# Kernel tuning notes

Hardware: AMD Instinct MI355X
Metric: run time of the kernel (lower is better)

Reference implementation:

```python
import jax, jax.numpy as jnp
import numpy as np

B, C, T = 4, 80, 800            # batch, n_mels (= d_model), frames
DEPTH, D_IN, N, DT_R, K = 12, 160, 16, 5, 4  # layers, expand*d_model, d_state, dt_rank, conv kernel
ATT, EMB, EPS = 128, 192, 1e-12

LP_NAMES = ['ln1_g','ln1_b','in_proj','conv_w','conv_b','x_proj','dt_w','dt_b','A_log','D','out_proj','ln2_g','ln2_b','ff_w1','ff_b1','ff_w2','ff_b2']
PP_NAMES = ['att_w1','att_b1','bn1_g','bn1_b','bn1_m','bn1_v','att_w2','att_b2','bn2_g','bn2_b','bn2_m','bn2_v','fc_w','fc_b']


def _layernorm(x, g, b, eps=1e-5):
    mu = x.mean(-1, keepdims=True)
    v = ((x - mu) ** 2).mean(-1, keepdims=True)
    return (x - mu) * jax.lax.rsqrt(v + eps) * g + b


def _mamba(x, p):
    # x: [B, L, d_model] -> standard Mamba selective-scan block
    xz = x @ p['in_proj']                              # [B,L,2*D_IN]
    xc, z = jnp.split(xz, 2, axis=-1)
    xp = jnp.pad(xc, ((0, 0), (K - 1, 0), (0, 0)))     # causal left pad
    xc = jax.lax.conv_general_dilated(
        xp, p['conv_w'], (1,), 'VALID',
        dimension_numbers=('NWC', 'WIO', 'NWC'),
        feature_group_count=D_IN) + p['conv_b']
    xc = jax.nn.silu(xc)
    dbc = xc @ p['x_proj']                             # [B,L,DT_R+2N]
    dt, Bm, Cm = jnp.split(dbc, [DT_R, DT_R + N], axis=-1)
    dt = jax.nn.softplus(dt @ p['dt_w'] + p['dt_b'])   # [B,L,D_IN]
    A = -jnp.exp(p['A_log'])                           # [D_IN,N]

    def step(h, inp):
        x_t, dt_t, B_t, C_t = inp                      # [B,D],[B,D],[B,N],[B,N]
        dA = jnp.exp(dt_t[..., None] * A)              # [B,D,N]
        h = dA * h + (dt_t * x_t)[..., None] * B_t[:, None, :]
        y = jnp.einsum('bdn,bn->bd', h, C_t)
        return h, y

    h0 = jnp.zeros((x.shape[0], D_IN, N), x.dtype)
    xs = tuple(jnp.swapaxes(a, 0, 1) for a in (xc, dt, Bm, Cm))
    _, ys = jax.lax.scan(step, h0, xs)
    y = jnp.swapaxes(ys, 0, 1) + xc * p['D']
    y = y * jax.nn.silu(z)
    return y @ p['out_proj']


def _encoder(x, p):
    xn = _layernorm(x, p['ln1_g'], p['ln1_b'])
    fwd = _mamba(xn, p)
    bwd = jnp.flip(_mamba(jnp.flip(xn, 1), p), 1)      # bidirectional, shared weights
    m = _layernorm(fwd + bwd, p['ln2_g'], p['ln2_b'])
    ff = jax.nn.gelu(m @ p['ff_w1'] + p['ff_b1'], approximate=False) @ p['ff_w2'] + p['ff_b2']
    return ff + x


def _forward(feat, lp, pp):
    feat = feat - feat.mean(-1, keepdims=True)         # CMN
    x = jnp.swapaxes(feat, 1, 2)                       # [B,T,C]

    def body(xc, p):
        return _encoder(xc, p), None

    x, _ = jax.lax.scan(body, x, lp)                   # 12 stacked layers
    x = jnp.swapaxes(x, 1, 2)                          # [B,C,T]

    # Attentive statistics pooling (global context)
    mean = x.mean(-1, keepdims=True)
    std = jnp.sqrt(jnp.maximum(((x - mean) ** 2).mean(-1, keepdims=True), EPS))
    g = jnp.concatenate([x, jnp.broadcast_to(mean, x.shape), jnp.broadcast_to(std, x.shape)], axis=1)  # [B,3C,T]
    a = jnp.einsum('bct,cd->bdt', g, pp['att_w1']) + pp['att_b1'][:, None]
    a = jax.nn.relu(a)
    a = (a - pp['bn1_m'][:, None]) * jax.lax.rsqrt(pp['bn1_v'][:, None] + 1e-5) * pp['bn1_g'][:, None] + pp['bn1_b'][:, None]
    a = jnp.tanh(a)
    a = jnp.einsum('bdt,dc->bct', a, pp['att_w2']) + pp['att_b2'][:, None]
    w = jax.nn.softmax(a, axis=-1)
    mu = jnp.sum(w * x, axis=-1)
    sg = jnp.sqrt(jnp.maximum(jnp.sum(w * x * x, axis=-1) - mu ** 2, EPS))
    pooled = jnp.concatenate([mu, sg], axis=-1)        # [B,2C]

    pooled = (pooled - pp['bn2_m']) * jax.lax.rsqrt(pp['bn2_v'] + 1e-5) * pp['bn2_g'] + pp['bn2_b']
    return pooled @ pp['fc_w'] + pp['fc_b']            # [B,EMB] source embedding


def setup_inputs() -> dict:
    key = jax.random.key(0)
    ks = jax.random.split(key, 12)

    def w(k, shape, s=0.05):
        return jax.random.normal(k, shape, jnp.float32) * s

    L = DEPTH
    return {
        'feat': jax.random.normal(ks[0], (B, C, T), jnp.float32),
        'ln1_g': jnp.ones((L, C)), 'ln1_b': jnp.zeros((L, C)),
        'in_proj': w(ks[1], (L, C, 2 * D_IN)),
        'conv_w': w(ks[2], (L, K, 1, D_IN), 0.2),
        'conv_b': jnp.zeros((L, D_IN)),
        'x_proj': w(ks[3], (L, D_IN, DT_R + 2 * N)),
        'dt_w': w(ks[4], (L, DT_R, D_IN), 0.2),
        'dt_b': jnp.full((L, D_IN), -2.0),
        'A_log': jnp.tile(jnp.log(jnp.arange(1, N + 1, dtype=jnp.float32)), (L, D_IN, 1)),
        'D': jnp.ones((L, D_IN)),
        'out_proj': w(ks[5], (L, D_IN, C)),
        'ln2_g': jnp.ones((L, C)), 'ln2_b': jnp.zeros((L, C)),
        'ff_w1': w(ks[6], (L, C, 4 * C)), 'ff_b1': jnp.zeros((L, 4 * C)),
        'ff_w2': w(ks[7], (L, 4 * C, C)), 'ff_b2': jnp.zeros((L, C)),
        'att_w1': w(ks[8], (3 * C, ATT)), 'att_b1': jnp.zeros((ATT,)),
        'bn1_g': jnp.ones((ATT,)), 'bn1_b': jnp.zeros((ATT,)),
        'bn1_m': jnp.zeros((ATT,)), 'bn1_v': jnp.ones((ATT,)),
        'att_w2': w(ks[9], (ATT, C)), 'att_b2': jnp.zeros((C,)),
        'bn2_g': jnp.ones((2 * C,)), 'bn2_b': jnp.zeros((2 * C,)),
        'bn2_m': jnp.zeros((2 * C,)), 'bn2_v': jnp.ones((2 * C,)),
        'fc_w': w(ks[10], (2 * C, EMB)), 'fc_b': jnp.zeros((EMB,)),
        'aug': 0,
    }


def reference(feat, ln1_g, ln1_b, in_proj, conv_w, conv_b, x_proj, dt_w, dt_b, A_log, D, out_proj, ln2_g, ln2_b, ff_w1, ff_b1, ff_w2, ff_b2, att_w1, att_b1, bn1_g, bn1_b, bn1_m, bn1_v, att_w2, att_b2, bn2_g, bn2_b, bn2_m, bn2_v, fc_w, fc_b, aug):
    lp = dict(zip(LP_NAMES, (ln1_g, ln1_b, in_proj, conv_w, conv_b, x_proj, dt_w, dt_b, A_log, D, out_proj, ln2_g, ln2_b, ff_w1, ff_b1, ff_w2, ff_b2)))
    pp = dict(zip(PP_NAMES, (att_w1, att_b1, bn1_g, bn1_b, bn1_m, bn1_v, att_w2, att_b2, bn2_g, bn2_b, bn2_m, bn2_v, fc_w, fc_b)))
    # aug == 0 -> SpecAug skipped (eval path); speaker branch (frozen, no_grad) omitted
    return _forward(feat, lp, pp)
```

## Files before the change

kernel.cpp:

```cpp
#include <hip/hip_runtime.h>
#include <hip/hip_bf16.h>

#define B_ 4
#define C_ 80
#define T_ 800
#define R_ 3200
#define DIN 160
#define NST 16
#define NC 16
#define LCH 50

typedef const float* fp;

__device__ __forceinline__ void g2l16(const float* g, float* l) {
  __builtin_amdgcn_global_load_lds(
      (const __attribute__((address_space(1))) void*)g,
      (__attribute__((address_space(3))) void*)l,
      16, 0, 0);
}

__device__ __forceinline__ float blockSum(float v, float* sb) {
  for (int o = 32; o; o >>= 1) v += __shfl_xor(v, o);
  __syncthreads();
  if ((threadIdx.x & 63) == 0) sb[threadIdx.x >> 6] = v;
  __syncthreads();
  return sb[0] + sb[1] + sb[2] + sb[3];
}
__device__ __forceinline__ float blockMax(float v, float* sb) {
  for (int o = 32; o; o >>= 1) v = fmaxf(v, __shfl_xor(v, o));
  __syncthreads();
  if ((threadIdx.x & 63) == 0) sb[threadIdx.x >> 6] = v;
  __syncthreads();
  return fmaxf(fmaxf(sb[0], sb[1]), fmaxf(sb[2], sb[3]));
}

__global__ __launch_bounds__(256) void prepw_k(fp in_proj, fp ff_w1,
    fp ln1_g, fp ln1_b, fp ln2_g, fp ln2_b, fp ff_b1,
    float* __restrict__ wp, float* __restrict__ uvb) {
  int idx = blockIdx.x * 256 + threadIdx.x;
  int c = idx % 320, lm = idx / 320;
  int mat = lm & 1, l = lm >> 1;
  fp W = (mat ? ff_w1 : in_proj) + l * 25600;
  fp g = (mat ? ln2_g : ln1_g) + l * 80;
  fp b = (mat ? ln2_b : ln1_b) + l * 80;
  float* wpo = wp + lm * 25600;
  float u = 0.f, v = 0.f;
  for (int k = 0; k < 80; ++k) {
    float w = W[k * 320 + c];
    float gw = g[k] * w;
    wpo[k * 320 + c] = gw;
    u += gw;
    v += b[k] * w;
  }
  if (mat) v += ff_b1[l * 320 + c];
  uvb[lm * 640 + c] = u;
  uvb[lm * 640 + 320 + c] = v;
}

__global__ __launch_bounds__(256) void prepx_k(fp x_proj, float* __restrict__ xpt) {
  int idx = blockIdx.x * 256 + threadIdx.x;
  if (idx >= 71040) return;
  int l = idx / 5920, r = idx % 5920;
  int c = r / 160, k = r % 160;
  xpt[idx] = x_proj[l * 5920 + k * 37 + c];
}

__global__ __launch_bounds__(256) void prept_k(fp out_proj, fp ff_w2,
    float* __restrict__ wot, float* __restrict__ w2t) {
  int idx = blockIdx.x * 256 + threadIdx.x;
  if (idx < 153600) {
    int l = idx / 12800, r = idx % 12800;
    int c = r / 160, k = r % 160;
    wot[idx] = out_proj[l * 12800 + k * 80 + c];
  } else if (idx < 153600 + 307200) {
    int j = idx - 153600;
    int l = j / 25600, r = j % 25600;
    int c = r / 320, k = r % 320;
    w2t[j] = ff_w2[l * 25600 + k * 80 + c];
  }
}

__global__ __launch_bounds__(256) void cmn_k(fp feat, float* __restrict__ x) {
  int bc = blockIdx.x;
  int b = bc / C_, c = bc % C_;
// ... 34 lines not shown
    float mu = s * 0.0125f;
    float rs = rsqrtf(fmaxf(q * 0.0125f - mu * mu, 0.f) + 1e-5f);
    must[row * 2] = mu;
    must[row * 2 + 1] = rs;
  }
}

template<int EPI>
__global__ __launch_bounds__(256, 4) void gw_k(const float* __restrict__ A,
    fp W, fp uv, const float* __restrict__ must, const float* __restrict__ extra,
    float* __restrict__ out, int N) {
  __shared__ float SL[5120 + 4 * 1280];
  int tid = threadIdx.x, wv = tid >> 6, ln = tid & 63;
  int bid = blockIdx.x;
  int c0 = (bid / 50) * 64;
  int row0 = ((bid % 50) * 4 + wv) * 16;
  for (int ch = wv; ch < 20; ch += 4) {
    int m = ch * 256 + ln * 4;
    int kr = m >> 6, cc = m & 63;
    int lo = __builtin_amdgcn_readfirstlane(ch * 256);
    g2l16(W + kr * N + c0 + cc, SL + lo);
  }
  int abase = __builtin_amdgcn_readfirstlane(5120 + wv * 1280);
  float* As = SL + 5120 + wv * 1280;
  #pragma unroll
  for (int i = 0; i < 5; ++i) {
    int m = i * 256 + ln * 4;
    int r = m / 80, kk = m - r * 80;
    g2l16(A + (row0 + r) * 80 + kk, SL + abase + i * 256);
  }
  __syncthreads();
  int rq = ln >> 4, c16 = ln & 15;
  float acc[4][4] = {};
  #pragma unroll 2
  for (int k4 = 0; k4 < 80; k4 += 4) {
    float4 a[4], w[4];
    #pragma unroll
    for (int i = 0; i < 4; ++i)
      a[i] = *(const float4*)&As[(rq * 4 + i) * 80 + k4];
    #pragma unroll
    for (int kk = 0; kk < 4; ++kk)
      w[kk] = *(const float4*)&SL[(k4 + kk) * 64 + c16 * 4];
    #pragma unroll
    for (int i = 0; i < 4; ++i) {
      acc[i][0] += a[i].x*w[0].x + a[i].y*w[1].x + a[i].z*w[2].x + a[i].w*w[3].x;
      acc[i][1] += a[i].x*w[0].y + a[i].y*w[1].y + a[i].z*w[2].y + a[i].w*w[3].y;
      acc[i][2] += a[i].x*w[0].z + a[i].y*w[1].z + a[i].z*w[2].z + a[i].w*w[3].z;
      acc[i][3] += a[i].x*w[0].w + a[i].y*w[1].w + a[i].z*w[2].w + a[i].w*w[3].w;
    }
  }
  float ua[4], va[4];
  if (EPI != 3) {
    *(float4*)ua = *(const float4*)&uv[c0 + c16 * 4];
    *(float4*)va = *(const float4*)&uv[N + c0 + c16 * 4];
  }
  #pragma unroll
  for (int i = 0; i < 4; ++i) {
    int row = row0 + rq * 4 + i;
    float mu = 0.f, rs = 1.f;
    if (EPI != 3) {
      float2 ms = *(const float2*)&must[row * 2];
      mu = ms.x; rs = ms.y;
    }
    float4 o;
    float* op = &o.x;
    #pragma unroll
    for (int j = 0; j < 4; ++j) {
      float v = acc[i][j];
      if (EPI == 3) {
        int c = c0 + c16 * 4 + j;
        v += extra[(row / T_) * 128 + c];
        v = fmaxf(v, 0.f);
        v = v * extra[512 + c] + extra[640 + c];
        v = tanhf(v);
      } else {
        v = rs * v - mu * rs * ua[j] + va[j];
      }
      op[j] = v;
    }
    *(float4*)&out[row * N + c0 + c16 * 4] = o;
  }
}

template<int EPI, int KCH, int NKC, int SUM2, int STAT>
__global__ __launch_bounds__(256, 4) void gc_k(const float* __restrict__ A,
    fp W, fp bias, const float* __restrict__ extra, float* __restrict__ out,
    int Astride, float* __restrict__ must) {
  constexpr int P = KCH + 4;
  __shared__ float As[16 * P];
  __shared__ float Wt[80 * P];
  int tid = threadIdx.x;
  int row0 = blockIdx.x * 16;
  int rr = tid >> 4, c16 = tid & 15;
  float acc[5] = {};
  for (int kc = 0; kc < NKC; ++kc) {
    if (kc) __syncthreads();
    #pragma unroll
    for (int i = 0; i < 16 * KCH / 256; ++i) {
      int e = tid + i * 256;
      int r = e / KCH, k = e - r * KCH;
      float v;
      if (SUM2) v = A[(row0 + r) * 320 + k] + A[(row0 + r) * 320 + 160 + k];
      else      v = A[(row0 + r) * Astride + kc * KCH + k];
      As[r * P + k] = v;
    }
    #pragma unroll
    for (int i = 0; i < KCH * 80 / 256; ++i) {
      int e = tid + i * 256;
      int kr = e / 80, c = e - kr * 80;
      Wt[c * P + kr] = W[(kc * KCH + kr) * 80 + c];
    }
    __syncthreads();
    #pragma unroll 4
    for (int k4 = 0; k4 < KCH; k4 += 4) {
      float4 a = *(const float4*)&As[rr * P + k4];
      #pragma unroll
      for (int m = 0; m < 5; ++m) {
        float4 w = *(const float4*)&Wt[(c16 + 16 * m) * P + k4];
        acc[m] += a.x * w.x + a.y * w.y + a.z * w.z + a.w * w.w;
      }
    }
  }
  int row = row0 + rr;
  #pragma unroll
  for (int m = 0; m < 5; ++m) {
    int c = c16 + 16 * m;
    float v = acc[m];
    if (EPI == 2) v += bias[c] + extra[row * 80 + c];
    else if (EPI == 4) v += bias[c];
    out[row * 80 + c] = v;
  }
}

__global__ __launch_bounds__(256, 2) void gof_k(const float* __restrict__ yg,
    fp wotl, fp w1pl, fp uv1, float* __restrict__ g1) {
  __shared__ float As[16 * 164];
  __shared__ float Wt[80 * 164];
  __shared__ float sl[16 * 84];
  __shared__ float ss[32];
  int tid = threadIdx.x, row0 = blockIdx.x * 16, rr = tid >> 4, c16 = tid & 15;
  #pragma unroll
  for (int i = 0; i < 10; ++i) {
    int e = tid + i * 256; int r = e / 160, k = e - r * 160;
    As[r * 164 + k] = yg[(row0 + r) * 320 + k] + yg[(row0 + r) * 320 + 160 + k];
  }
  #pragma unroll
  for (int i = 0; i < 50; ++i) {
    int e = tid + i * 256; int c = e / 160, k = e - c * 160;
    Wt[c * 164 + k] = wotl[e];
  }
  __syncthreads();
  float acc[5] = {};
  #pragma unroll 4
  for (int k4 = 0; k4 < 160; k4 += 4) {
    float4 a = *(const float4*)&As[rr * 164 + k4];
    #pragma unroll
    for (int m = 0; m < 5; ++m) {
      float4 w = *(const float4*)&Wt[(c16 + 16 * m) * 164 + k4];
      acc[m] += a.x * w.x + a.y * w.y + a.z * w.z + a.w * w.w;
    }
  }
  float s = 0.f, q = 0.f;
  #pragma unroll
  for (int m = 0; m < 5; ++m) {
    float v = acc[m];
    sl[rr * 84 + c16 + 16 * m] = v;
    s += v; q += v * v;
  }
  s += __shfl_xor(s, 1); s += __shfl_xor(s, 2);
  s += __shfl_xor(s, 4); s += __shfl_xor(s, 8);
  q += __shfl_xor(q, 1); q += __shfl_xor(q, 2);
  q += __shfl_xor(q, 4); q += __shfl_xor(q, 8);
  if (c16 == 0) {
    float mu = s * 0.0125f;
    ss[rr * 2] = mu;
    ss[rr * 2 + 1] = rsqrtf(fmaxf(q * 0.0125f - mu * mu, 0.f) + 1e-5f);
  }
  for (int h = 0; h < 2; ++h) {
    __syncthreads();
    #pragma unroll
    for (int i = 0; i < 50; ++i) {
      int e = tid + i * 256; int kr = e / 160, c = e - kr * 160;
      Wt[kr * 164 + c] = w1pl[kr * 320 + h * 160 + c];
    }
    __syncthreads();
    float mu = ss[rr * 2], rs = ss[rr * 2 + 1];
    float a2[10] = {};
    for (int k = 0; k < 80; k += 4) {
      float4 av = *(const float4*)&sl[rr * 84 + k];
      #pragma unroll
      for (int m = 0; m < 10; ++m) {
        int c = c16 + 16 * m;
        a2[m] += av.x * Wt[k * 164 + c] + av.y * Wt[(k + 1) * 164 + c]
               + av.z * Wt[(k + 2) * 164 + c] + av.w * Wt[(k + 3) * 164 + c];
      }
    }
    #pragma unroll
    for (int m = 0; m < 10; ++m) {
      int c = h * 160 + c16 + 16 * m;
      float v = rs * a2[m] - mu * rs * uv1[c] + uv1[320 + c];
      v = 0.5f * v * (1.f + erff(v * 0.70710678118f));
      g1[(row0 + rr) * 320 + c] = v;
    }
  }
}

template<int LAST>
__global__ __launch_bounds__(256, 2) void gfi_k(const float* __restrict__ g1,
    fp w2tl, fp fb2, float* __restrict__ x, fp wpn, fp uvn,
    float* __restrict__ xz) {
  __shared__ float As[16 * 164];
  __shared__ float Wt[80 * 164];
  __shared__ float xn[16 * 84];
  __shared__ float ss[32];
  int tid = threadIdx.x, row0 = blockIdx.x * 16, rr = tid >> 4, c16 = tid & 15;
  float acc[5] = {};
  for (int kc = 0; kc < 2; ++kc) {
    if (kc) __syncthreads();
    #pragma unroll
    for (int i = 0; i < 10; ++i) {
      int e = tid + i * 256; int r = e / 160, k = e - r * 160;
      As[r * 164 + k] = g1[(row0 + r) * 320 + kc * 160 + k];
    }
    #pragma unroll
    for (int i = 0; i < 50; ++i) {
      int e = tid + i * 256; int c = e / 160, k = e - c * 160;
      Wt[c * 164 + k] = w2tl[c * 320 + kc * 160 + k];
    }
    __syncthreads();
    #pragma unroll 4
    for (int k4 = 0; k4 < 160; k4 += 4) {
      float4 a = *(const float4*)&As[rr * 164 + k4];
      #pragma unroll
      for (int m = 0; m < 5; ++m) {
        float4 w = *(const float4*)&Wt[(c16 + 16 * m) * 164 + k4];
        acc[m] += a.x * w.x + a.y * w.y + a.z * w.z + a.w * w.w;
      }
    }
  }
  float s = 0.f, q = 0.f;
  #pragma unroll
  for (int m = 0; m < 5; ++m) {
    int c = c16 + 16 * m;
    float v = acc[m] + fb2[c] + x[(row0 + rr) * 80 + c];
    x[(row0 + rr) * 80 + c] = v;
    xn[rr * 84 + c] = v;
    s += v; q += v * v;
  }
  if (!LAST) {
    s += __shfl_xor(s, 1); s += __shfl_xor(s, 2);
    s += __shfl_xor(s, 4); s += __shfl_xor(s, 8);
    q += __shfl_xor(q, 1); q += __shfl_xor(q, 2);
    q += __shfl_xor(q, 4); q += __shfl_xor(q, 8);
    if (c16 == 0) {
      float mu = s * 0.0125f;
      ss[rr * 2] = mu;
      ss[rr * 2 + 1] = rsqrtf(fmaxf(q * 0.0125f - mu * mu, 0.f) + 1e-5f);
    }
    for (int h = 0; h < 2; ++h) {
      __syncthreads();
      #pragma unroll
      for (int i = 0; i < 50; ++i) {
        int e = tid + i * 256; int kr = e / 160, c = e - kr * 160;
        Wt[kr * 164 + c] = wpn[kr * 320 + h * 160 + c];
      }
      __syncthreads();
      float mu = ss[rr * 2], rs = ss[rr * 2 + 1];
      float a2[10] = {};
      for (int k = 0; k < 80; k += 4) {
        float4 av = *(const float4*)&xn[rr * 84 + k];
        #pragma unroll
        for (int m = 0; m < 10; ++m) {
          int c = c16 + 16 * m;
          a2[m] += av.x * Wt[k * 164 + c] + av.y * Wt[(k + 1) * 164 + c]
                 + av.z * Wt[(k + 2) * 164 + c] + av.w * Wt[(k + 3) * 164 + c];
        }
      }
      #pragma unroll
      for (int m = 0; m < 10; ++m) {
        int c = h * 160 + c16 + 16 * m;
        xz[(row0 + rr) * 320 + c] = rs * a2[m] - mu * rs * uvn[c] + uvn[320 + c];
      }
    }
  }
}

__global__ __launch_bounds__(256) void cxf_k(const float* __restrict__ xz,
    fp cw, fp cb, fp xptl, fp dtw, fp dtb,
    float* __restrict__ xcf, float* __restrict__ xcbb,
    float* __restrict__ dbc2, float* __restrict__ dt2) {
  __shared__ float As[16 * 164];
  __shared__ float xpT[37 * 164];
  __shared__ float dbcl[16 * 40];
  int bi = blockIdx.x;
  int tc = bi % 50; int rem = bi / 50;
  int b = rem & 3, dir = rem >> 2;
  int t0 = tc * 16;
  int tid = threadIdx.x;
  #pragma unroll
  for (int i = 0; i < 24; ++i) {
    int e = tid + i * 256;
    if (e < 5920) {
      int c = e / 160, k = e - c * 160;
      xpT[c * 164 + k] = xptl[e];
    }
  }
  float* xco = dir ? xcbb : xcf;
  #pragma unroll
  for (int i = 0; i < 3; ++i) {
    int e = tid + i * 256;
    if (e < 640) {
      int ii = e / 40, d4 = (e - ii * 40) * 4;
      int t = t0 + ii;
      float4 acc = *(const float4*)&cb[d4];
      #pragma unroll
      for (int k = 0; k < 4; ++k) {
        int tt = t - 3 + k;
        if (tt >= 0) {
          int src = dir ? (T_ - 1 - tt) : tt;
          float4 xv = *(const float4*)&xz[(b * T_ + src) * 320 + d4];
          float4 wv = *(const float4*)&cw[k * DIN + d4];
          acc.x += wv.x * xv.x; acc.y += wv.y * xv.y;
          acc.z += wv.z * xv.z; acc.w += wv.w * xv.w;
        }
      }
      float4 o;
      o.x = acc.x / (1.f + __expf(-acc.x));
      o.y = acc.y / (1.f + __expf(-acc.y));
      o.z = acc.z / (1.f + __expf(-acc.z));
      o.w = acc.w / (1.f + __expf(-acc.w));
      *(float4*)&As[ii * 164 + d4] = o;
      *(float4*)&xco[(b * T_ + t) * DIN + d4] = o;
    }
  }
  __syncthreads();
  int rr = tid >> 4, c16 = tid & 15;
  int grow0 = dir * R_ + b * T_ + t0;
  {
    float a0 = 0.f, a1 = 0.f, a2 = 0.f;
    for (int k4 = 0; k4 < 160; k4 += 4) {
      float4 a = *(const float4*)&As[rr * 164 + k4];
      float4 w0 = *(const float4*)&xpT[c16 * 164 + k4];
      float4 w1 = *(const float4*)&xpT[(c16 + 16) * 164 + k4];
      a0 += a.x * w0.x + a.y * w0.y + a.z * w0.z + a.w * w0.w;
      a1 += a.x * w1.x + a.y * w1.y + a.z * w1.z + a.w * w1.w;
      if (c16 < 5) {
        float4 w2 = *(const float4*)&xpT[(c16 + 32) * 164 + k4];
        a2 += a.x * w2.x + a.y * w2.y + a.z * w2.z + a.w * w2.w;
      }
    }
    dbcl[rr * 40 + c16] = a0;
    dbcl[rr * 40 + c16 + 16] = a1;
    dbc2[(grow0 + rr) * 37 + c16] = a0;
    dbc2[(grow0 + rr) * 37 + c16 + 16] = a1;
    if (c16 < 5) {
      dbcl[rr * 40 + c16 + 32] = a2;
      dbc2[(grow0 + rr) * 37 + c16 + 32] = a2;
    }
  }
  __syncthreads();
  #pragma unroll
  for (int i = 0; i < 10; ++i) {
    int e = tid + i * 256;
    int ii = e / 160, d = e - ii * 160;
    float v = dtb[d];
    #pragma unroll
    for (int m = 0; m < 5; ++m) v += dbcl[ii * 40 + m] * dtw[m * DIN + d];
    v = fmaxf(v, 0.f) + __logf(1.f + __expf(-fabsf(v)));
    dt2[(grow0 + ii) * DIN + d] = v;
  }
}

__global__ __launch_bounds__(256) void scanA_k(const float* __restrict__ dt2,
    const float* __restrict__ xcf, const float* __restrict__ xcbb,
    const float* __restrict__ dbc2, fp A_log,
    float* __restrict__ hend, float* __restrict__ pprod) {
  int bi = blockIdx.x;
  int cch = bi % NC; int rem = bi / NC;
  int dblk = rem % 10; rem /= 10;
  int b = rem % 4; int dir = rem / 4;
  int d0 = dblk * 16;
  int tid = threadIdx.x, dl = tid >> 4, n = tid & 15;
  int d = d0 + dl;
  float Areg = -__expf(A_log[d * NST + n]);
  __shared__ float sdt[LCH][16], sdx[LCH][16], sB[LCH][16];
  const float* xc = dir ? xcbb : xcf;
  int rbase = dir * R_ + b * T_ + cch * LCH;
  int rloc0 = b * T_ + cch * LCH;
  for (int e = tid; e < LCH * 16; e += 256) {
    int i = e >> 4, jj = e & 15;
    int grow = rbase + i;
    float dtv = dt2[grow * DIN + d0 + jj];
    sdt[i][jj] = dtv;
    sdx[i][jj] = dtv * xc[(rloc0 + i) * DIN + d0 + jj];
    sB[i][jj]  = dbc2[grow * 37 + 5 + jj];
  }
  __syncthreads();
  float h = 0.f, dts = 0.f;
  #pragma unroll 2
  for (int i = 0; i < LCH; ++i) {
    float dtv = sdt[i][dl];
    float a = __expf(dtv * Areg);
    h = a * h + sdx[i][dl] * sB[i][n];
    dts += dtv;
  }
  hend[bi * 256 + tid] = h;
  pprod[bi * 256 + tid] = __expf(dts * Areg);
}

__global__ __launch_bounds__(256) void scanC_k(const float* __restrict__ dt2,
    const float* __restrict__ dbc2, const float* __restrict__ xcf,
    const float* __restrict__ xcbb, const float* __restrict__ xz,
    fp A_log, fp Dp, const float* __restrict__ hend,
    const float* __restrict__ pprod, float* __restrict__ ygcat) {
  int bi = blockIdx.x;
  int cch = bi % NC; int rem = bi / NC;
  int dblk = rem % 10; rem /= 10;
  int b = rem % 4; int dir = rem / 4;
  int d0 = dblk * 16;
  int tid = threadIdx.x, dl = tid >> 4, n = tid & 15;
  int d = d0 + dl;
  float Areg = -__expf(A_log[d * NST + n]);
  __shared__ float sdt[LCH][16], sdx[LCH][16], sB[LCH][16], sC[LCH][16];
  __shared__ float sY[LCH][16];
  const float* xc = dir ? xcbb : xcf;
  int rbase = dir * R_ + b * T_ + cch * LCH;
  int rloc0 = b * T_ + cch * LCH;
  int sbase = (bi / NC) * (NC * 256) + tid;
  float h = 0.f;
  #pragma unroll
  for (int cc = 0; cc < NC; ++cc) {
    float p = pprod[sbase + cc * 256];
    float e = hend[sbase + cc * 256];
    if (cc < cch) h = p * h + e;
  }
  for (int e = tid; e < LCH * 16; e += 256) {
    int i = e >> 4, jj = e & 15;
    int grow = rbase + i;
    float dtv = dt2[grow * DIN + d0 + jj];
    sdt[i][jj] = dtv;
    sdx[i][jj] = dtv * xc[(rloc0 + i) * DIN + d0 + jj];
    sB[i][jj]  = dbc2[grow * 37 + 5 + jj];
    sC[i][jj]  = dbc2[grow * 37 + 21 + jj];
  }
  __syncthreads();
  for (int i = 0; i < LCH; ++i) {
    float a = __expf(sdt[i][dl] * Areg);
    h = a * h + sdx[i][dl] * sB[i][n];
    float y = h * sC[i][n];
    y += __shfl_xor(y, 1);
    y += __shfl_xor(y, 2);
    y += __shfl_xor(y, 4);
    y += __shfl_xor(y, 8);
    if (n == 0) sY[i][dl] = y;
  }
  __syncthreads();
  for (int e = tid; e < LCH * 16; e += 256) {
    int i = e >> 4, jj = e & 15;
    int t = cch * LCH + i;
    int rloc = b * T_ + t;
    float xcv = xc[rloc * DIN + d0 + jj];
    int orow = dir ? (b * T_ + (T_ - 1 - t)) : rloc;
    float z = xz[orow * 320 + 160 + d0 + jj];
    float sg = 1.f / (1.f + __expf(-z));
    ygcat[orow * 320 + dir * 160 + d0 + jj] = (sY[i][jj] + xcv * Dp[d0 + jj]) * (z * sg);
  }
}

__global__ __launch_bounds__(256) void stats_k(const float* __restrict__ x,
                                               float* __restrict__ meanv, float* __restrict__ stdv) {
  int bc = blockIdx.x; int b = bc / C_, c = bc % C_;
  __shared__ float sb[4];
  int tid = threadIdx.x;
  float v[4]; float s = 0.f;
  #pragma unroll
  for (int i = 0; i < 4; ++i) {
    int t = tid + i * 256;
    v[i] = (t < T_) ? x[(b * T_ + t) * C_ + c] : 0.f;
    s += v[i];
  }
  s = blockSum(s, sb);
  float mu = s * (1.f / T_);
  float q = 0.f;
  #pragma unroll
  for (int i = 0; i < 4; ++i) {
    int t = tid + i * 256;
    if (t < T_) { float dd = v[i] - mu; q += dd * dd; }
  }
  q = blockSum(q, sb);
  if (tid == 0) { meanv[bc] = mu; stdv[bc] = sqrtf(fmaxf(q * (1.f / T_), 1e-12f)); }
}

__global__ __launch_bounds__(256) void prep_k(const float* __restrict__ meanv,
    const float* __restrict__ stdv, fp w1, fp ab1, fp g1p, fp b1p, fp m1p, fp v1p,
    float* __restrict__ pack) {
  int idx = blockIdx.x * 256 + threadIdx.x;
  if (idx < 512) {
    int b = idx / 128, dcol = idx % 128;
    float acc = ab1[dcol];
    for (int c = 0; c < C_; ++c) {
      acc += meanv[b * C_ + c] * w1[(C_ + c) * 128 + dcol];
      acc += stdv[b * C_ + c] * w1[(2 * C_ + c) * 128 + dcol];
    }
    pack[idx] = acc;
  } else if (idx < 640) {
    int dcol = idx - 512;
    float kv = g1p[dcol] * rsqrtf(v1p[dcol] + 1e-5f);
    pack[512 + dcol] = kv;
    pack[640 + dcol] = b1p[dcol] - m1p[dcol] * kv;
  }
}

__global__ __launch_bounds__(256) void pool_k(const float* __restrict__ x,
    const float* __restrict__ scores, fp g2, fp b2, fp m2, fp v2,
    float* __restrict__ pooledn) {
  int bc = blockIdx.x; int b = bc / C_, c = bc % C_;
  __shared__ float sb[4];
  int tid = threadIdx.x;
  float sv[4], xv[4];
  float mx = -1e30f;
  #pragma unroll
  for (int i = 0; i < 4; ++i) {
    int t = tid + i * 256;
    if (t < T_) { sv[i] = scores[(b * T_ + t) * C_ + c]; xv[i] = x[(b * T_ + t) * C_ + c]; }
    else { sv[i] = -1e30f; xv[i] = 0.f; }
    mx = fmaxf(mx, sv[i]);
  }
  mx = blockMax(mx, sb);
  float se = 0.f, sx = 0.f, sxx = 0.f;
  #pragma unroll
  for (int i = 0; i < 4; ++i) {
    float e = expf(sv[i] - mx);
    se += e; sx += e * xv[i]; sxx += e * xv[i] * xv[i];
  }
  se = blockSum(se, sb);
  sx = blockSum(sx, sb);
  sxx = blockSum(sxx, sb);
  if (tid == 0) {
    float mu = sx / se;
    float sg = sqrtf(fmaxf(sxx / se - mu * mu, 1e-12f));
    int j0 = c, j1 = C_ + c;
    pooledn[b * 160 + j0] = (mu - m2[j0]) * rsqrtf(v2[j0] + 1e-5f) * g2[j0] + b2[j0];
    pooledn[b * 160 + j1] = (sg - m2[j1]) * rsqrtf(v2[j1] + 1e-5f) * g2[j1] + b2[j1];
  }
}

__global__ __launch_bounds__(256) void fc_k(const float* __restrict__ pooledn, fp fw, fp fb,
                                            float* __restrict__ out) {
  int idx = blockIdx.x * 256 + threadIdx.x;
  if (idx >= 4 * 192) return;
  int b = idx / 192, e = idx % 192;
  float acc = fb[e];
  for (int i = 0; i < 160; ++i) acc += pooledn[b * 160 + i] * fw[i * 192 + e];
  out[idx] = acc;
}

extern "C" void kernel_launch(void* const* d_in, const int* in_sizes, int n_in,
                              void* d_out, int out_size, void* d_ws, size_t ws_size,
                              hipStream_t stream) {
  fp feat   = (fp)d_in[0];
  fp ln1_g  = (fp)d_in[1];  fp ln1_b  = (fp)d_in[2];
  fp in_proj= (fp)d_in[3];
  fp conv_w = (fp)d_in[4];  fp conv_b = (fp)d_in[5];
  fp x_proj = (fp)d_in[6];
  fp dt_w   = (fp)d_in[7];  fp dt_b   = (fp)d_in[8];
  fp A_log  = (fp)d_in[9];  fp Dp     = (fp)d_in[10];
  fp out_proj=(fp)d_in[11];
  fp ln2_g  = (fp)d_in[12]; fp ln2_b  = (fp)d_in[13];
  fp ff_w1  = (fp)d_in[14]; fp ff_b1  = (fp)d_in[15];
  fp ff_w2  = (fp)d_in[16]; fp ff_b2  = (fp)d_in[17];
  fp att_w1 = (fp)d_in[18]; fp att_b1 = (fp)d_in[19];
  fp bn1_g  = (fp)d_in[20]; fp bn1_b  = (fp)d_in[21];
  fp bn1_m  = (fp)d_in[22]; fp bn1_v  = (fp)d_in[23];
  fp att_w2 = (fp)d_in[24]; fp att_b2 = (fp)d_in[25];
  fp bn2_g  = (fp)d_in[26]; fp bn2_b  = (fp)d_in[27];
  fp bn2_m  = (fp)d_in[28]; fp bn2_v  = (fp)d_in[29];
  fp fc_w   = (fp)d_in[30]; fp fc_b   = (fp)d_in[31];

  float* ws   = (float*)d_ws;
  float* x    = ws;
  float* xz   = ws + 256000;
  float* xcf  = ws + 1280000;
  float* xcb  = ws + 1792000;
  float* dbc2 = ws + 2304000;
  float* dt2  = ws + 2540800;
  float* hend = ws + 3564800;
  float* pprod= ws + 3892480;
  float* ygcat= ws + 4220160;
  float* meanv= ws + 5244160;
  float* stdv = ws + 5244480;
  float* pack = ws + 5244800;
  float* pooledn = ws + 5245568;
  float* wp   = ws + 5246208;
  float* uvb  = ws + 5860608;
  float* mst_x= ws + 5875968;
  float* xpt  = ws + 5882368;
  float* wot  = ws + 5953408;
  float* w2t  = ws + 6107008;
  float* g1   = xz;
  float* a1b  = hend;
  float* sc   = dt2;

  prepw_k<<<30, 256, 0, stream>>>(in_proj, ff_w1, ln1_g, ln1_b, ln2_g, ln2_b,
                                  ff_b1, wp, uvb);
  prepx_k<<<278, 256, 0, stream>>>(x_proj, xpt);
  prept_k<<<1800, 256, 0, stream>>>(out_proj, ff_w2, wot, w2t);
  cmn_k<<<320, 256, 0, stream>>>(feat, x);
  rstat_k<<<200, 256, 0, stream>>>(x, mst_x);
  gw_k<0><<<250, 256, 0, stream>>>(x, wp, uvb, mst_x, nullptr, xz, 320);

  for (int l = 0; l < 12; ++l) {
    cxf_k<<<400, 256, 0, stream>>>(xz, conv_w + l * 640, conv_b + l * 160,
                                   xpt + l * 5920, dt_w + l * 800, dt_b + l * 160,
                                   xcf, xcb, dbc2, dt2);
    scanA_k<<<1280, 256, 0, stream>>>(dt2, xcf, xcb, dbc2, A_log + l * 2560, hend, pprod);
    scanC_k<<<1280, 256, 0, stream>>>(dt2, dbc2, xcf, xcb, xz, A_log + l * 2560,
                                      Dp + l * 160, hend, pprod, ygcat);
    gof_k<<<200, 256, 0, stream>>>(ygcat, wot + l * 12800, wp + (2 * l + 1) * 25600,
                                   uvb + (2 * l + 1) * 640, g1);
    if (l < 11)
      gfi_k<0><<<200, 256, 0, stream>>>(g1, w2t + l * 25600, ff_b2 + l * 80, x,
                                        wp + (2 * l + 2) * 25600,
                                        uvb + (2 * l + 2) * 640, xz);
    else
      gfi_k<1><<<200, 256, 0, stream>>>(g1, w2t + l * 25600, ff_b2 + l * 80, x,
                                        wp, uvb, xz);
  }

  stats_k<<<320, 256, 0, stream>>>(x, meanv, stdv);
  prep_k<<<3, 256, 0, stream>>>(meanv, stdv, att_w1, att_b1, bn1_g, bn1_b, bn1_m, bn1_v, pack);
  gw_k<3><<<100, 256, 0, stream>>>(x, att_w1, nullptr, nullptr, pack, a1b, 128);
  gc_k<4, 128, 1, 0, 0><<<200, 256, 0, stream>>>(a1b, att_w2, att_b2, nullptr, sc, 128, nullptr);
  pool_k<<<320, 256, 0, stream>>>(x, sc, bn2_g, bn2_b, bn2_m, bn2_v, pooledn);
  fc_k<<<3, 256, 0, stream>>>(pooledn, fc_w, fc_b, (float*)d_out);
}
```

Measured before the change: 1.262 ms.

## Fuse per-layer encoder kernels into a persistent cooperative megakernel with grid syncs

Replaces the five per-layer kernel launches (conv/x_proj, two scan passes, out-projection and FFN stages) across 12 layers with one cooperative persistent kernel of 400 blocks. Grid-wide barriers separate the phases, and the scan work items are strided over the resident blocks. The aim is to remove launch gaps and inter-kernel drain and fill overhead. In exchange, the scans run with fewer concurrent blocks and a single large LDS allocation, and a fallback path with separate kernels is kept for when the cooperative launch fails.

```diff
diff --git a/kernel.cpp b/kernel.cpp
--- a/kernel.cpp
+++ b/kernel.cpp
@@ -1,5 +1,8 @@
 #include <hip/hip_runtime.h>
 #include <hip/hip_bf16.h>
+#include <hip/hip_cooperative_groups.h>
+
+namespace cg = cooperative_groups;
 
 #define B_ 4
 #define C_ 80
@@ -200,10 +203,9 @@
   }
 }
 
-template<int EPI, int KCH, int NKC, int SUM2, int STAT>
+template<int EPI, int KCH, int NKC>
 __global__ __launch_bounds__(256, 4) void gc_k(const float* __restrict__ A,
-    fp W, fp bias, const float* __restrict__ extra, float* __restrict__ out,
-    int Astride, float* __restrict__ must) {
+    fp W, fp bias, float* __restrict__ out, int Astride) {
   constexpr int P = KCH + 4;
   __shared__ float As[16 * P];
   __shared__ float Wt[80 * P];
@@ -217,10 +219,7 @@
     for (int i = 0; i < 16 * KCH / 256; ++i) {
       int e = tid + i * 256;
       int r = e / KCH, k = e - r * KCH;
-      float v;
-      if (SUM2) v = A[(row0 + r) * 320 + k] + A[(row0 + r) * 320 + 160 + k];
-      else      v = A[(row0 + r) * Astride + kc * KCH + k];
-      As[r * P + k] = v;
+      As[r * P + k] = A[(row0 + r) * Astride + kc * KCH + k];
     }
     #pragma unroll
     for (int i = 0; i < KCH * 80 / 256; ++i) {
@@ -244,173 +243,19 @@
   for (int m = 0; m < 5; ++m) {
     int c = c16 + 16 * m;
     float v = acc[m];
-    if (EPI == 2) v += bias[c] + extra[row * 80 + c];
-    else if (EPI == 4) v += bias[c];
+    if (EPI == 4) v += bias[c];
     out[row * 80 + c] = v;
   }
 }
 
-__global__ __launch_bounds__(256, 2) void gof_k(const float* __restrict__ yg,
-    fp wotl, fp w1pl, fp uv1, float* __restrict__ g1) {
-  __shared__ float As[16 * 164];
-  __shared__ float Wt[80 * 164];
-  __shared__ float sl[16 * 84];
-  __shared__ float ss[32];
-  int tid = threadIdx.x, row0 = blockIdx.x * 16, rr = tid >> 4, c16 = tid & 15;
-  #pragma unroll
-  for (int i = 0; i < 10; ++i) {
-    int e = tid + i * 256; int r = e / 160, k = e - r * 160;
-    As[r * 164 + k] = yg[(row0 + r) * 320 + k] + yg[(row0 + r) * 320 + 160 + k];
-  }
-  #pragma unroll
-  for (int i = 0; i < 50; ++i) {
-    int e = tid + i * 256; int c = e / 160, k = e - c * 160;
-    Wt[c * 164 + k] = wotl[e];
-  }
-  __syncthreads();
-  float acc[5] = {};
-  #pragma unroll 4
-  for (int k4 = 0; k4 < 160; k4 += 4) {
-    float4 a = *(const float4*)&As[rr * 164 + k4];
-    #pragma unroll
-    for (int m = 0; m < 5; ++m) {
-      float4 w = *(const float4*)&Wt[(c16 + 16 * m) * 164 + k4];
-      acc[m] += a.x * w.x + a.y * w.y + a.z * w.z + a.w * w.w;
-    }
-  }
-  float s = 0.f, q = 0.f;
-  #pragma unroll
-  for (int m = 0; m < 5; ++m) {
-    float v = acc[m];
-    sl[rr * 84 + c16 + 16 * m] = v;
-    s += v; q += v * v;
-  }
-  s += __shfl_xor(s, 1); s += __shfl_xor(s, 2);
-  s += __shfl_xor(s, 4); s += __shfl_xor(s, 8);
-  q += __shfl_xor(q, 1); q += __shfl_xor(q, 2);
-  q += __shfl_xor(q, 4); q += __shfl_xor(q, 8);
-  if (c16 == 0) {
-    float mu = s * 0.0125f;
-    ss[rr * 2] = mu;
-    ss[rr * 2 + 1] = rsqrtf(fmaxf(q * 0.0125f - mu * mu, 0.f) + 1e-5f);
-  }
-  for (int h = 0; h < 2; ++h) {
-    __syncthreads();
-    #pragma unroll
-    for (int i = 0; i < 50; ++i) {
-      int e = tid + i * 256; int kr = e / 160, c = e - kr * 160;
-      Wt[kr * 164 + c] = w1pl[kr * 320 + h * 160 + c];
-    }
-    __syncthreads();
-    float mu = ss[rr * 2], rs = ss[rr * 2 + 1];
-    float a2[10] = {};
-    for (int k = 0; k < 80; k += 4) {
-      float4 av = *(const float4*)&sl[rr * 84 + k];
-      #pragma unroll
-      for (int m = 0; m < 10; ++m) {
-        int c = c16 + 16 * m;
-        a2[m] += av.x * Wt[k * 164 + c] + av.y * Wt[(k + 1) * 164 + c]
-               + av.z * Wt[(k + 2) * 164 + c] + av.w * Wt[(k + 3) * 164 + c];
-      }
-    }
-    #pragma unroll
-    for (int m = 0; m < 10; ++m) {
-      int c = h * 160 + c16 + 16 * m;
-      float v = rs * a2[m] - mu * rs * uv1[c] + uv1[320 + c];
-      v = 0.5f * v * (1.f + erff(v * 0.70710678118f));
-      g1[(row0 + rr) * 320 + c] = v;
-    }
-  }
-}
-
-template<int LAST>
-__global__ __launch_bounds__(256, 2) void gfi_k(const float* __restrict__ g1,
-    fp w2tl, fp fb2, float* __restrict__ x, fp wpn, fp uvn,
-    float* __restrict__ xz) {
-  __shared__ float As[16 * 164];
-  __shared__ float Wt[80 * 164];
-  __shared__ float xn[16 * 84];
-  __shared__ float ss[32];
-  int tid = threadIdx.x, row0 = blockIdx.x * 16, rr = tid >> 4, c16 = tid & 15;
-  float acc[5] = {};
-  for (int kc = 0; kc < 2; ++kc) {
-    if (kc) __syncthreads();
-    #pragma unroll
-    for (int i = 0; i < 10; ++i) {
-      int e = tid + i * 256; int r = e / 160, k = e - r * 160;
-      As[r * 164 + k] = g1[(row0 + r) * 320 + kc * 160 + k];
-    }
-    #pragma unroll
-    for (int i = 0; i < 50; ++i) {
-      int e = tid + i * 256; int c = e / 160, k = e - c * 160;
-      Wt[c * 164 + k] = w2tl[c * 320 + kc * 160 + k];
-    }
-    __syncthreads();
-    #pragma unroll 4
-    for (int k4 = 0; k4 < 160; k4 += 4) {
-      float4 a = *(const float4*)&As[rr * 164 + k4];
-      #pragma unroll
-      for (int m = 0; m < 5; ++m) {
-        float4 w = *(const float4*)&Wt[(c16 + 16 * m) * 164 + k4];
-        acc[m] += a.x * w.x + a.y * w.y + a.z * w.z + a.w * w.w;
-      }
-    }
-  }
-  float s = 0.f, q = 0.f;
-  #pragma unroll
-  for (int m = 0; m < 5; ++m) {
-    int c = c16 + 16 * m;
-    float v = acc[m] + fb2[c] + x[(row0 + rr) * 80 + c];
-    x[(row0 + rr) * 80 + c] = v;
-    xn[rr * 84 + c] = v;
-    s += v; q += v * v;
-  }
-  if (!LAST) {
-    s += __shfl_xor(s, 1); s += __shfl_xor(s, 2);
-    s += __shfl_xor(s, 4); s += __shfl_xor(s, 8);
-    q += __shfl_xor(q, 1); q += __shfl_xor(q, 2);
-    q += __shfl_xor(q, 4); q += __shfl_xor(q, 8);
-    if (c16 == 0) {
-      float mu = s * 0.0125f;
-      ss[rr * 2] = mu;
-      ss[rr * 2 + 1] = rsqrtf(fmaxf(q * 0.0125f - mu * mu, 0.f) + 1e-5f);
-    }
-    for (int h = 0; h < 2; ++h) {
-      __syncthreads();
-      #pragma unroll
-      for (int i = 0; i < 50; ++i) {
-        int e = tid + i * 256; int kr = e / 160, c = e - kr * 160;
-        Wt[kr * 164 + c] = wpn[kr * 320 + h * 160 + c];
-      }
-      __syncthreads();
-      float mu = ss[rr * 2], rs = ss[rr * 2 + 1];
-      float a2[10] = {};
-      for (int k = 0; k < 80; k += 4) {
-        float4 av = *(const float4*)&xn[rr * 84 + k];
-        #pragma unroll
-        for (int m = 0; m < 10; ++m) {
-          int c = c16 + 16 * m;
-          a2[m] += av.x * Wt[k * 164 + c] + av.y * Wt[(k + 1) * 164 + c]
-                 + av.z * Wt[(k + 2) * 164 + c] + av.w * Wt[(k + 3) * 164 + c];
-        }
-      }
-      #pragma unroll
-      for (int m = 0; m < 10; ++m) {
-        int c = h * 160 + c16 + 16 * m;
-        xz[(row0 + rr) * 320 + c] = rs * a2[m] - mu * rs * uvn[c] + uvn[320 + c];
-      }
-    }
-  }
-}
-
-__global__ __launch_bounds__(256) void cxf_k(const float* __restrict__ xz,
-    fp cw, fp cb, fp xptl, fp dtw, fp dtb,
-    float* __restrict__ xcf, float* __restrict__ xcbb,
-    float* __restrict__ dbc2, float* __restrict__ dt2) {
-  __shared__ float As[16 * 164];
-  __shared__ float xpT[37 * 164];
-  __shared__ float dbcl[16 * 40];
-  int bi = blockIdx.x;
+
+__device__ void cxf_dev(float* S, int bi, const float* xz, const float* cw,
+                        const float* cb, const float* xptl, const float* dtw,
+                        const float* dtb, float* xcf, float* xcbb,
+                        float* dbc2, float* dt2) {
+  float* As   = S;
+  float* xpT  = S + 2624;
+  float* dbcl = S + 8692;
   int tc = bi % 50; int rem = bi / 50;
   int b = rem & 3, dir = rem >> 2;
   int t0 = tc * 16;
@@ -489,11 +334,10 @@
   }
 }
 
-__global__ __launch_bounds__(256) void scanA_k(const float* __restrict__ dt2,
-    const float* __restrict__ xcf, const float* __restrict__ xcbb,
-    const float* __restrict__ dbc2, fp A_log,
-    float* __restrict__ hend, float* __restrict__ pprod) {
-  int bi = blockIdx.x;
+__device__ void scanA_dev(float* S, int bi, const float* dt2, const float* xcf,
+                          const float* xcbb, const float* dbc2, const float* A_log,
+                          float* hend, float* pprod) {
+  float* sdt = S; float* sdx = S + 800; float* sB = S + 1600;
   int cch = bi % NC; int rem = bi / NC;
   int dblk = rem % 10; rem /= 10;
   int b = rem % 4; int dir = rem / 4;
@@ -501,7 +345,6 @@
   int tid = threadIdx.x, dl = tid >> 4, n = tid & 15;
   int d = d0 + dl;
   float Areg = -__expf(A_log[d * NST + n]);
-  __shared__ float sdt[LCH][16], sdx[LCH][16], sB[LCH][16];
   const float* xc = dir ? xcbb : xcf;
   int rbase = dir * R_ + b * T_ + cch * LCH;
   int rloc0 = b * T_ + cch * LCH;
@@ -509,29 +352,29 @@
     int i = e >> 4, jj = e & 15;
     int grow = rbase + i;
     float dtv = dt2[grow * DIN + d0 + jj];
-    sdt[i][jj] = dtv;
-    sdx[i][jj] = dtv * xc[(rloc0 + i) * DIN + d0 + jj];
-    sB[i][jj]  = dbc2[grow * 37 + 5 + jj];
+    sdt[i * 16 + jj] = dtv;
+    sdx[i * 16 + jj] = dtv * xc[(rloc0 + i) * DIN + d0 + jj];
+    sB[i * 16 + jj]  = dbc2[grow * 37 + 5 + jj];
   }
   __syncthreads();
   float h = 0.f, dts = 0.f;
   #pragma unroll 2
   for (int i = 0; i < LCH; ++i) {
-    float dtv = sdt[i][dl];
-    float a = __expf(dtv * Areg);
-    h = a * h + sdx[i][dl] * sB[i][n];
+    float dtv = sdt[i * 16 + dl];
+    float aa = __expf(dtv * Areg);
+    h = aa * h + sdx[i * 16 + dl] * sB[i * 16 + n];
     dts += dtv;
   }
   hend[bi * 256 + tid] = h;
   pprod[bi * 256 + tid] = __expf(dts * Areg);
 }
 
-__global__ __launch_bounds__(256) void scanC_k(const float* __restrict__ dt2,
-    const float* __restrict__ dbc2, const float* __restrict__ xcf,
-    const float* __restrict__ xcbb, const float* __restrict__ xz,
-    fp A_log, fp Dp, const float* __restrict__ hend,
-    const float* __restrict__ pprod, float* __restrict__ ygcat) {
-  int bi = blockIdx.x;
+__device__ void scanC_dev(float* S, int bi, const float* dt2, const float* dbc2,
+                          const float* xcf, const float* xcbb, const float* xz,
+                          const float* A_log, const float* Dp,
+                          const float* hend, const float* pprod, float* ygcat) {
+  float* sdt = S; float* sdx = S + 800; float* sB = S + 1600;
+  float* sC = S + 2400; float* sY = S + 3200;
   int cch = bi % NC; int rem = bi / NC;
   int dblk = rem % 10; rem /= 10;
   int b = rem % 4; int dir = rem / 4;
@@ -539,8 +382,6 @@
   int tid = threadIdx.x, dl = tid >> 4, n = tid & 15;
   int d = d0 + dl;
   float Areg = -__expf(A_log[d * NST + n]);
-  __shared__ float sdt[LCH][16], sdx[LCH][16], sB[LCH][16], sC[LCH][16];
-  __shared__ float sY[LCH][16];
   const float* xc = dir ? xcbb : xcf;
   int rbase = dir * R_ + b * T_ + cch * LCH;
   int rloc0 = b * T_ + cch * LCH;
@@ -556,21 +397,21 @@
     int i = e >> 4, jj = e & 15;
     int grow = rbase + i;
     float dtv = dt2[grow * DIN + d0 + jj];
-    sdt[i][jj] = dtv;
-    sdx[i][jj] = dtv * xc[(rloc0 + i) * DIN + d0 + jj];
-    sB[i][jj]  = dbc2[grow * 37 + 5 + jj];
-    sC[i][jj]  = dbc2[grow * 37 + 21 + jj];
+    sdt[i * 16 + jj] = dtv;
+    sdx[i * 16 + jj] = dtv * xc[(rloc0 + i) * DIN + d0 + jj];
+    sB[i * 16 + jj]  = dbc2[grow * 37 + 5 + jj];
+    sC[i * 16 + jj]  = dbc2[grow * 37 + 21 + jj];
   }
   __syncthreads();
   for (int i = 0; i < LCH; ++i) {
-    float a = __expf(sdt[i][dl] * Areg);
-    h = a * h + sdx[i][dl] * sB[i][n];
-    float y = h * sC[i][n];
+    float a = __expf(sdt[i * 16 + dl] * Areg);
+    h = a * h + sdx[i * 16 + dl] * sB[i * 16 + n];
+    float y = h * sC[i * 16 + n];
     y += __shfl_xor(y, 1);
     y += __shfl_xor(y, 2);
     y += __shfl_xor(y, 4);
     y += __shfl_xor(y, 8);
-    if (n == 0) sY[i][dl] = y;
+    if (n == 0) sY[i * 16 + dl] = y;
   }
   __syncthreads();
   for (int e = tid; e < LCH * 16; e += 256) {
@@ -581,8 +422,232 @@
     int orow = dir ? (b * T_ + (T_ - 1 - t)) : rloc;
     float z = xz[orow * 320 + 160 + d0 + jj];
     float sg = 1.f / (1.f + __expf(-z));
-    ygcat[orow * 320 + dir * 160 + d0 + jj] = (sY[i][jj] + xcv * Dp[d0 + jj]) * (z * sg);
-  }
+    ygcat[orow * 320 + dir * 160 + d0 + jj] = (sY[i * 16 + jj] + xcv * Dp[d0 + jj]) * (z * sg);
+  }
+}
+
+__device__ void gof_dev(float* S, int bid, const float* yg, const float* wotl,
+                        const float* w1pl, const float* uv1, float* g1) {
+  float* Wt = S;
+  float* As = S + 13120;
+  float* sl = S + 15744;
+  float* ss = S + 17088;
+  int tid = threadIdx.x, row0 = bid * 16, rr = tid >> 4, c16 = tid & 15;
+  #pragma unroll
+  for (int i = 0; i < 10; ++i) {
+    int e = tid + i * 256; int r = e / 160, k = e - r * 160;
+    As[r * 164 + k] = yg[(row0 + r) * 320 + k] + yg[(row0 + r) * 320 + 160 + k];
+  }
+  #pragma unroll
+  for (int i = 0; i < 50; ++i) {
+    int e = tid + i * 256; int c = e / 160, k = e - c * 160;
+    Wt[c * 164 + k] = wotl[e];
+  }
+  __syncthreads();
+  {
+    float acc[5] = {};
+    #pragma unroll 4
+    for (int k4 = 0; k4 < 160; k4 += 4) {
+      float4 a = *(const float4*)&As[rr * 164 + k4];
+      #pragma unroll
+      for (int m = 0; m < 5; ++m) {
+        float4 w = *(const float4*)&Wt[(c16 + 16 * m) * 164 + k4];
+        acc[m] += a.x * w.x + a.y * w.y + a.z * w.z + a.w * w.w;
+      }
+    }
+    float s = 0.f, q = 0.f;
+    #pragma unroll
+    for (int m = 0; m < 5; ++m) {
+      float v = acc[m];
+      sl[rr * 84 + c16 + 16 * m] = v;
+      s += v; q += v * v;
+    }
+    s += __shfl_xor(s, 1); s += __shfl_xor(s, 2);
+    s += __shfl_xor(s, 4); s += __shfl_xor(s, 8);
+    q += __shfl_xor(q, 1); q += __shfl_xor(q, 2);
+    q += __shfl_xor(q, 4); q += __shfl_xor(q, 8);
+    if (c16 == 0) {
+      float mu = s * 0.0125f;
+      ss[rr * 2] = mu;
+      ss[rr * 2 + 1] = rsqrtf(fmaxf(q * 0.0125f - mu * mu, 0.f) + 1e-5f);
+    }
+  }
+  for (int h = 0; h < 2; ++h) {
+    __syncthreads();
+    #pragma unroll
+    for (int i = 0; i < 50; ++i) {
+      int e = tid + i * 256; int kr = e / 160, c = e - kr * 160;
+      Wt[kr * 164 + c] = w1pl[kr * 320 + h * 160 + c];
+    }
+    __syncthreads();
+    float mu = ss[rr * 2], rs = ss[rr * 2 + 1];
+    float a2[10] = {};
+    for (int k = 0; k < 80; k += 4) {
+      float4 av = *(const float4*)&sl[rr * 84 + k];
+      #pragma unroll
+      for (int m = 0; m < 10; ++m) {
+        int c = c16 + 16 * m;
+        a2[m] += av.x * Wt[k * 164 + c] + av.y * Wt[(k + 1) * 164 + c]
+               + av.z * Wt[(k + 2) * 164 + c] + av.w * Wt[(k + 3) * 164 + c];
+      }
+    }
+    #pragma unroll
+    for (int m = 0; m < 10; ++m) {
+      int c = h * 160 + c16 + 16 * m;
+      float v = rs * a2[m] - mu * rs * uv1[c] + uv1[320 + c];
+      v = 0.5f * v * (1.f + erff(v * 0.70710678118f));
+      g1[(row0 + rr) * 320 + c] = v;
+    }
+  }
+}
+
+__device__ void gfi_dev(float* S, int bid, const float* g1, const float* w2tl,
+                        const float* fb2, float* x, const float* wpn,
+                        const float* uvn, float* xz, int last) {
+  float* Wt = S;
+  float* As = S + 13120;
+  float* xn = S + 15744;
+  float* ss = S + 17088;
+  int tid = threadIdx.x, row0 = bid * 16, rr = tid >> 4, c16 = tid & 15;
+  float acc2[5] = {};
+  for (int kc = 0; kc < 2; ++kc) {
+    if (kc) __syncthreads();
+    #pragma unroll
+    for (int i = 0; i < 10; ++i) {
+      int e = tid + i * 256; int r = e / 160, k = e - r * 160;
+      As[r * 164 + k] = g1[(row0 + r) * 320 + kc * 160 + k];
+    }
+    #pragma unroll
+    for (int i = 0; i < 50; ++i) {
+      int e = tid + i * 256; int c = e / 160, k = e - c * 160;
+      Wt[c * 164 + k] = w2tl[c * 320 + kc * 160 + k];
+    }
+    __syncthreads();
+    #pragma unroll 4
+    for (int k4 = 0; k4 < 160; k4 += 4) {
+      float4 a = *(const float4*)&As[rr * 164 + k4];
+      #pragma unroll
+      for (int m = 0; m < 5; ++m) {
+        float4 w = *(const float4*)&Wt[(c16 + 16 * m) * 164 + k4];
+        acc2[m] += a.x * w.x + a.y * w.y + a.z * w.z + a.w * w.w;
+      }
+    }
+  }
+  {
+    float s = 0.f, q = 0.f;
+    #pragma unroll
+    for (int m = 0; m < 5; ++m) {
+      int c = c16 + 16 * m;
+      float v = acc2[m] + fb2[c] + x[(row0 + rr) * 80 + c];
+      x[(row0 + rr) * 80 + c] = v;
+      xn[rr * 84 + c] = v;
+      s += v; q += v * v;
+    }
+    if (!last) {
+      s += __shfl_xor(s, 1); s += __shfl_xor(s, 2);
+      s += __shfl_xor(s, 4); s += __shfl_xor(s, 8);
+      q += __shfl_xor(q, 1); q += __shfl_xor(q, 2);
+      q += __shfl_xor(q, 4); q += __shfl_xor(q, 8);
+      if (c16 == 0) {
+        float mu = s * 0.0125f;
+        ss[rr * 2] = mu;
+        ss[rr * 2 + 1] = rsqrtf(fmaxf(q * 0.0125f - mu * mu, 0.f) + 1e-5f);
+      }
+    }
+  }
+  if (!last) {
+    for (int h = 0; h < 2; ++h) {
+      __syncthreads();
+      #pragma unroll
+      for (int i = 0; i < 50; ++i) {
+        int e = tid + i * 256; int kr = e / 160, c = e - kr * 160;
+        Wt[kr * 164 + c] = wpn[kr * 320 + h * 160 + c];
+      }
+      __syncthreads();
+      float mu = ss[rr * 2], rs = ss[rr * 2 + 1];
+      float a3[10] = {};
+      for (int k = 0; k < 80; k += 4) {
+        float4 av = *(const float4*)&xn[rr * 84 + k];
+        #pragma unroll
+        for (int m = 0; m < 10; ++m) {
+          int c = c16 + 16 * m;
+          a3[m] += av.x * Wt[k * 164 + c] + av.y * Wt[(k + 1) * 164 + c]
+                 + av.z * Wt[(k + 2) * 164 + c] + av.w * Wt[(k + 3) * 164 + c];
+        }
+      }
+      #pragma unroll
+      for (int m = 0; m < 10; ++m) {
+        int c = h * 160 + c16 + 16 * m;
+        xz[(row0 + rr) * 320 + c] = rs * a3[m] - mu * rs * uvn[c] + uvn[320 + c];
+      }
+    }
+  }
+}
+
+struct MA {
+  const float *xpt, *conv_w, *conv_b, *dt_w, *dt_b, *A_log, *Dp;
+  const float *wp, *uvb, *wot, *w2t, *ff_b2;
+  float *x, *xz, *xcf, *xcb, *dbc2, *dt2, *hend, *pprod, *ygcat;
+};
+
+__global__ __launch_bounds__(256, 2) void mega_k(MA a) {
+  __shared__ float S[17120];
+  cg::grid_group gg = cg::this_grid();
+  int bid = blockIdx.x;
+  for (int l = 0; l < 12; ++l) {
+    cxf_dev(S, bid, a.xz, a.conv_w + l * 640, a.conv_b + l * 160,
+            a.xpt + l * 5920, a.dt_w + l * 800, a.dt_b + l * 160,
+            a.xcf, a.xcb, a.dbc2, a.dt2);
+    gg.sync();
+    for (int u = bid; u < 1280; u += 400) {
+      scanA_dev(S, u, a.dt2, a.xcf, a.xcb, a.dbc2, a.A_log + l * 2560,
+                a.hend, a.pprod);
+      __syncthreads();
+    }
+    gg.sync();
+    for (int u = bid; u < 1280; u += 400) {
+      scanC_dev(S, u, a.dt2, a.dbc2, a.xcf, a.xcb, a.xz, a.A_log + l * 2560,
+                a.Dp + l * 160, a.hend, a.pprod, a.ygcat);
+      __syncthreads();
+    }
+    gg.sync();
+    if (bid < 200) {
+      gof_dev(S, bid, a.ygcat, a.wot + l * 12800, a.wp + (2 * l + 1) * 25600,
+              a.uvb + (2 * l + 1) * 640, a.xz);
+      __syncthreads();
+      int nl = (l < 11) ? (2 * l + 2) : 0;
+      gfi_dev(S, bid, a.xz, a.w2t + l * 25600, a.ff_b2 + l * 80, a.x,
+              a.wp + nl * 25600, a.uvb + nl * 640, a.xz, l == 11);
+    }
+    gg.sync();
+  }
+}
+
+__global__ __launch_bounds__(256, 2) void cxf_g(const float* xz, fp cw, fp cb,
+    fp xptl, fp dtw, fp dtb, float* xcf, float* xcb, float* dbc2, float* dt2) {
+  __shared__ float S[9332];
+  cxf_dev(S, blockIdx.x, xz, cw, cb, xptl, dtw, dtb, xcf, xcb, dbc2, dt2);
+}
+__global__ __launch_bounds__(256, 2) void scanA_g(const float* dt2, const float* xcf,
+    const float* xcb, const float* dbc2, fp A_log, float* hend, float* pprod) {
+  __shared__ float S[2400];
+  scanA_dev(S, blockIdx.x, dt2, xcf, xcb, dbc2, A_log, hend, pprod);
+}
+__global__ __launch_bounds__(256, 2) void scanC_g(const float* dt2, const float* dbc2,
+    const float* xcf, const float* xcb, const float* xz, fp A_log, fp Dp,
+    const float* hend, const float* pprod, float* ygcat) {
+  __shared__ float S[4000];
+  scanC_dev(S, blockIdx.x, dt2, dbc2, xcf, xcb, xz, A_log, Dp, hend, pprod, ygcat);
+}
+__global__ __launch_bounds__(256, 2) void gof_g(const float* yg, fp wotl, fp w1pl,
+    fp uv1, float* g1) {
+  __shared__ float S[17120];
+  gof_dev(S, blockIdx.x, yg, wotl, w1pl, uv1, g1);
+}
+__global__ __launch_bounds__(256, 2) void gfi_g(const float* g1, fp w2tl, fp fb2,
+    float* x, fp wpn, fp uvn, float* xz, int last) {
+  __shared__ float S[17120];
+  gfi_dev(S, blockIdx.x, g1, w2tl, fb2, x, wpn, uvn, xz, last);
 }
 
 __global__ __launch_bounds__(256) void stats_k(const float* __restrict__ x,
@@ -715,7 +780,6 @@
   float* xpt  = ws + 5882368;
   float* wot  = ws + 5953408;
   float* w2t  = ws + 6107008;
-  float* g1   = xz;
   float* a1b  = hend;
   float* sc   = dt2;
 
@@ -727,28 +791,39 @@
   rstat_k<<<200, 256, 0, stream>>>(x, mst_x);
   gw_k<0><<<250, 256, 0, stream>>>(x, wp, uvb, mst_x, nullptr, xz, 320);
 
-  for (int l = 0; l < 12; ++l) {
-    cxf_k<<<400, 256, 0, stream>>>(xz, conv_w + l * 640, conv_b + l * 160,
-                                   xpt + l * 5920, dt_w + l * 800, dt_b + l * 160,
-                                   xcf, xcb, dbc2, dt2);
-    scanA_k<<<1280, 256, 0, stream>>>(dt2, xcf, xcb, dbc2, A_log + l * 2560, hend, pprod);
-    scanC_k<<<1280, 256, 0, stream>>>(dt2, dbc2, xcf, xcb, xz, A_log + l * 2560,
-                                      Dp + l * 160, hend, pprod, ygcat);
-    gof_k<<<200, 256, 0, stream>>>(ygcat, wot + l * 12800, wp + (2 * l + 1) * 25600,
-                                   uvb + (2 * l + 1) * 640, g1);
-    if (l < 11)
-      gfi_k<0><<<200, 256, 0, stream>>>(g1, w2t + l * 25600, ff_b2 + l * 80, x,
-                                        wp + (2 * l + 2) * 25600,
-                                        uvb + (2 * l + 2) * 640, xz);
-    else
-      gfi_k<1><<<200, 256, 0, stream>>>(g1, w2t + l * 25600, ff_b2 + l * 80, x,
-                                        wp, uvb, xz);
+  MA ma;
+  ma.xpt = xpt; ma.conv_w = conv_w; ma.conv_b = conv_b;
+  ma.dt_w = dt_w; ma.dt_b = dt_b; ma.A_log = A_log; ma.Dp = Dp;
+  ma.wp = wp; ma.uvb = uvb; ma.wot = wot; ma.w2t = w2t; ma.ff_b2 = ff_b2;
+  ma.x = x; ma.xz = xz; ma.xcf = xcf; ma.xcb = xcb;
+  ma.dbc2 = dbc2; ma.dt2 = dt2; ma.hend = hend; ma.pprod = pprod;
+  ma.ygcat = ygcat;
+  void* kargs[] = { &ma };
+  hipError_t err = hipLaunchCooperativeKernel((void*)mega_k, dim3(400), dim3(256),
+                                              kargs, 0, stream);
+  if (err != hipSuccess) {
+    for (int l = 0; l < 12; ++l) {
+      cxf_g<<<400, 256, 0, stream>>>(xz, conv_w + l * 640, conv_b + l * 160,
+                                     xpt + l * 5920, dt_w + l * 800, dt_b + l * 160,
+                                     xcf, xcb, dbc2, dt2);
+      scanA_g<<<1280, 256, 0, stream>>>(dt2, xcf, xcb, dbc2, A_log + l * 2560,
+                                        hend, pprod);
+      scanC_g<<<1280, 256, 0, stream>>>(dt2, dbc2, xcf, xcb, xz, A_log + l * 2560,
+                                        Dp + l * 160, hend, pprod, ygcat);
+      gof_g<<<200, 256, 0, stream>>>(ygcat, wot + l * 12800,
+                                     wp + (2 * l + 1) * 25600,
+                                     uvb + (2 * l + 1) * 640, xz);
+      int nl = (l < 11) ? (2 * l + 2) : 0;
+      gfi_g<<<200, 256, 0, stream>>>(xz, w2t + l * 25600, ff_b2 + l * 80, x,
+                                     wp + nl * 25600, uvb + nl * 640, xz,
+                                     l == 11 ? 1 : 0);
+    }
   }
 
   stats_k<<<320, 256, 0, stream>>>(x, meanv, stdv);
   prep_k<<<3, 256, 0, stream>>>(meanv, stdv, att_w1, att_b1, bn1_g, bn1_b, bn1_m, bn1_v, pack);
   gw_k<3><<<100, 256, 0, stream>>>(x, att_w1, nullptr, nullptr, pack, a1b, 128);
-  gc_k<4, 128, 1, 0, 0><<<200, 256, 0, stream>>>(a1b, att_w2, att_b2, nullptr, sc, 128, nullptr);
+  gc_k<4, 128, 1><<<200, 256, 0, stream>>>(a1b, att_w2, att_b2, sc, 128);
   pool_k<<<320, 256, 0, stream>>>(x, sc, bn2_g, bn2_b, bn2_m, bn2_v, pooledn);
   fc_k<<<3, 256, 0, stream>>>(pooledn, fc_w, fc_b, (float*)d_out);
 }
```

Result: slower. 5.013 ms (+297.4%).
